# Kernel optimization log

Hardware: AMD Instinct MI355X
Metric: run time of the kernel (lower is better)

Reference implementation:

```python
import jax, jax.numpy as jnp
import numpy as np
import math

B, H, W, C = 8, 112, 112, 192
WS, SHIFT, NH = 7, 3, 6
HD = C // NH
N = WS * WS
NW = (H // WS) * (W // WS)
MLP_HID = 4 * C
LOG100 = math.log(100.0)


def _rel_table():
    ch = np.arange(-(WS - 1), WS, dtype=np.float32)
    t = np.stack(np.meshgrid(ch, ch, indexing='ij')).transpose(1, 2, 0).reshape(-1, 2)
    t = t / float(WS - 1) * 8.0
    t = np.sign(t) * np.log2(np.abs(t) + 1.0) / np.log2(8.0)
    return t.astype(np.float32)  # ((2*WS-1)^2, 2)


def _rel_index():
    coords = np.stack(np.meshgrid(np.arange(WS), np.arange(WS), indexing='ij')).reshape(2, -1)
    rel = (coords[:, :, None] - coords[:, None, :]).transpose(1, 2, 0)
    rel = rel + np.array([WS - 1, WS - 1])
    rel = rel * np.array([2 * WS - 1, 1])
    return rel.sum(-1).astype(np.int32)  # (N, N)


def _attn_mask():
    img = np.zeros((H, W), dtype=np.float32)
    cnt = 0
    for hsl in (slice(0, -WS), slice(-WS, -SHIFT), slice(-SHIFT, None)):
        for wsl in (slice(0, -WS), slice(-WS, -SHIFT), slice(-SHIFT, None)):
            img[hsl, wsl] = cnt
            cnt += 1
    mw = img.reshape(H // WS, WS, W // WS, WS).transpose(0, 2, 1, 3).reshape(-1, N)
    diff = mw[:, None, :] - mw[:, :, None]
    return np.where(diff != 0, -100.0, 0.0).astype(np.float32)  # (NW, N, N)

REL_TABLE = jnp.asarray(_rel_table())
REL_INDEX = jnp.asarray(_rel_index())
ATTN_MASK = jnp.asarray(_attn_mask())


def _ln(v, g, b, eps=1e-5):
    m = jnp.mean(v, axis=-1, keepdims=True)
    s = jnp.mean((v - m) ** 2, axis=-1, keepdims=True)
    return (v - m) / jnp.sqrt(s + eps) * g + b


def setup_inputs() -> dict:
    key = jax.random.key(0)
    ks = jax.random.split(key, 12)
    std = 0.02
    inp = {
        'x': jax.random.normal(ks[0], (B, H * W, C), jnp.float32),
        'q_w': jax.random.normal(ks[1], (C, C), jnp.float32) * std,
        'q_b': jnp.zeros((C,), jnp.float32),
        'k_w': jax.random.normal(ks[2], (C, C), jnp.float32) * std,
        'v_w': jax.random.normal(ks[3], (C, C), jnp.float32) * std,
        'v_b': jnp.zeros((C,), jnp.float32),
        'proj_w': jax.random.normal(ks[4], (C, C), jnp.float32) * std,
        'proj_b': jnp.zeros((C,), jnp.float32),
        'logit_scale': jnp.log(10.0 * jnp.ones((NH, 1, 1), jnp.float32)),
        'cpb_w0': jax.random.normal(ks[5], (2, 512), jnp.float32) * std,
        'cpb_b0': jnp.zeros((512,), jnp.float32),
        'cpb_w1': jax.random.normal(ks[6], (512, NH), jnp.float32) * std,
        'ln1_g': jnp.ones((C,), jnp.float32),
        'ln1_b': jnp.zeros((C,), jnp.float32),
        'ln2_g': jnp.ones((C,), jnp.float32),
        'ln2_b': jnp.zeros((C,), jnp.float32),
        'fc1_w': jax.random.normal(ks[7], (C, MLP_HID), jnp.float32) * std,
        'fc1_b': jnp.zeros((MLP_HID,), jnp.float32),
        'fc2_w': jax.random.normal(ks[8], (MLP_HID, C), jnp.float32) * std,
        'fc2_b': jnp.zeros((C,), jnp.float32),
    }
    return inp


def reference(x, q_w, q_b, k_w, v_w, v_b, proj_w, proj_b, logit_scale,
              cpb_w0, cpb_b0, cpb_w1, ln1_g, ln1_b, ln2_g, ln2_b,
              fc1_w, fc1_b, fc2_w, fc2_b):
    shortcut = x  # (B, L, C)
    h = x.reshape(B, H, W, C)
    # cyclic shift
    h = jnp.roll(h, shift=(-SHIFT, -SHIFT), axis=(1, 2))
    # window partition -> (B*NW, N, C)
    h = h.reshape(B, H // WS, WS, W // WS, WS, C).transpose(0, 1, 3, 2, 4, 5)
    h = h.reshape(B * NW, N, C)

    q = (h @ q_w + q_b).reshape(-1, N, NH, HD).transpose(0, 2, 1, 3)
    k = (h @ k_w).reshape(-1, N, NH, HD).transpose(0, 2, 1, 3)
    v = (h @ v_w + v_b).reshape(-1, N, NH, HD).transpose(0, 2, 1, 3)

    # cosine-similarity attention
    q = q / jnp.maximum(jnp.linalg.norm(q, axis=-1, keepdims=True), 1e-6)
    k = k / jnp.maximum(jnp.linalg.norm(k, axis=-1, keepdims=True), 1e-6)
    scale = jnp.exp(jnp.minimum(logit_scale, LOG100))  # (NH,1,1)
    attn = jnp.einsum('bhqd,bhkd->bhqk', q, k) * scale

    # relative position bias via CPB MLP
    rpb = jax.nn.relu(REL_TABLE @ cpb_w0 + cpb_b0) @ cpb_w1  # (169, NH)
    rpb = rpb[REL_INDEX.reshape(-1)].reshape(N, N, NH).transpose(2, 0, 1)
    rpb = 16.0 * jax.nn.sigmoid(rpb)  # (NH, N, N)
    attn = attn + rpb[None]

    # shift mask
    attn = attn.reshape(B, NW, NH, N, N) + ATTN_MASK[None, :, None]
    attn = attn.reshape(B * NW, NH, N, N)
    attn = jax.nn.softmax(attn, axis=-1)

    out = jnp.einsum('bhqk,bhkd->bhqd', attn, v)
    out = out.transpose(0, 2, 1, 3).reshape(B * NW, N, C)
    out = out @ proj_w + proj_b

    # window reverse + reverse shift
    out = out.reshape(B, H // WS, W // WS, WS, WS, C).transpose(0, 1, 3, 2, 4, 5)
    out = out.reshape(B, H, W, C)
    out = jnp.roll(out, shift=(SHIFT, SHIFT), axis=(1, 2)).reshape(B, H * W, C)

    # post-norm residual (Swin-v2)
    h1 = shortcut + _ln(out, ln1_g, ln1_b)
    mlp = jax.nn.gelu(h1 @ fc1_w + fc1_b) @ fc2_w + fc2_b
    return h1 + _ln(mlp, ln2_g, ln2_b)
```

## Files before the change

### kernel.cpp

```cpp
#include <hip/hip_runtime.h>

typedef unsigned short u16;
typedef unsigned int   u32;
typedef __attribute__((ext_vector_type(8))) short bf16x8;
typedef __attribute__((ext_vector_type(4))) float f32x4;

#define B_      8
#define HW_     112
#define C_      192
#define NH_     6
#define HD_     32
#define L_      (HW_*HW_)
#define M_      (B_*L_)
#define MLP_    768
#define QKVN_   576
#define LOG100_ 4.6051702f
#define LOG2E_  1.44269504f

__device__ __forceinline__ float bf2f(u16 u){
  union { float f; u32 i; } v; v.i = ((u32)u) << 16; return v.f;
}
__device__ __forceinline__ u16 f2bf(float f){
  union { float f; u32 i; } v; v.f = f;
  u32 r = (v.i + 0x7fffu + ((v.i >> 16) & 1u)) >> 16;
  return (u16)r;
}
__device__ __forceinline__ u32 cvtpk(float a, float b){
  u32 r;
  asm("v_cvt_pk_bf16_f32 %0, %1, %2" : "=v"(r) : "v"(a), "v"(b));
  return r;
}
__device__ __forceinline__ void u4_to_f8(uint4 u, float* f){
  f[0]=bf2f((u16)(u.x&0xffffu)); f[1]=bf2f((u16)(u.x>>16));
  f[2]=bf2f((u16)(u.y&0xffffu)); f[3]=bf2f((u16)(u.y>>16));
  f[4]=bf2f((u16)(u.z&0xffffu)); f[5]=bf2f((u16)(u.z>>16));
  f[6]=bf2f((u16)(u.w&0xffffu)); f[7]=bf2f((u16)(u.w>>16));
}

__device__ __forceinline__ int rowelem(int b, int wh, int ww, int t){
  int i = t/7, j = t - i*7;
  int oi = wh*7 + i + 3; if (oi >= 112) oi -= 112;
  int oj = ww*7 + j + 3; if (oj >= 112) oj -= 112;
  return b*L_ + oi*112 + oj;
}

__global__ __launch_bounds__(256) void prep_weights(
    const float* __restrict__ qw, const float* __restrict__ qb,
    const float* __restrict__ kw, const float* __restrict__ vw,
    const float* __restrict__ vb, const float* __restrict__ pw,
    const float* __restrict__ pb, const float* __restrict__ f1w,
    const float* __restrict__ f1b, const float* __restrict__ f2w,
    const float* __restrict__ f2b,
    u16* __restrict__ wt_qkv, float* __restrict__ b_qkv,
    u16* __restrict__ wt_p,   float* __restrict__ b_p,
    u16* __restrict__ wt_f1,  float* __restrict__ b_f1,
    u16* __restrict__ wt_f2,  float* __restrict__ b_f2)
{
  const int S1 = 110592, S2 = 147456, S3 = 294912, S4 = 442368, TOT = 444096;
  int i = blockIdx.x*256 + threadIdx.x;
  if (i >= TOT) return;
  if (i < S1) {
    int n = i/192, k = i%192;
    float v = (n<192) ? qw[k*192+n] : ((n<384) ? kw[k*192+(n-192)] : vw[k*192+(n-384)]);
    wt_qkv[i] = f2bf(v);
  } else if (i < S2) {
    int j = i - S1; int n = j/192, k = j%192;
    wt_p[j] = f2bf(pw[k*192+n]);
  } else if (i < S3) {
    int j = i - S2; int n = j/192, k = j%192;
    wt_f1[j] = f2bf(f1w[k*768+n]);
  } else if (i < S4) {
    int j = i - S3; int n = j/768, k = j%768;
    wt_f2[j] = f2bf(f2w[k*192+n]);
  } else {
    int j = i - S4;
    if (j < 576)        b_qkv[j] = (j<192) ? qb[j] : ((j<384) ? 0.f : vb[j-384]);
    else if (j < 768)   b_p[j-576]   = pb[j-576];
    else if (j < 1536)  b_f1[j-768]  = f1b[j-768];
    else                b_f2[j-1536] = f2b[j-1536];
  }
}

__device__ __forceinline__ float reltab(float x){
  float v = x * (8.f/6.f);
  float r = __log2f(fabsf(v) + 1.f) * (1.f/3.f);
  return (v < 0.f) ? -r : r;
}

__global__ __launch_bounds__(64) void rpb_a_kernel(
    const float* __restrict__ w0, const float* __restrict__ b0,
    const float* __restrict__ w1, float* __restrict__ rpb169)
{
  int tt = blockIdx.x, lane = threadIdx.x;
  float t0 = reltab((float)(tt/13 - 6));
  float t1 = reltab((float)(tt%13 - 6));
  float acc[6] = {0.f,0.f,0.f,0.f,0.f,0.f};
  for (int j = lane; j < 512; j += 64){
    float hid = fmaxf(t0*w0[j] + t1*w0[512+j] + b0[j], 0.f);
#pragma unroll
    for (int h=0; h<6; h++) acc[h] += hid * w1[j*6+h];
  }
#pragma unroll
  for (int h=0; h<6; h++){
#pragma unroll
    for (int m=32; m>=1; m>>=1) acc[h] += __shfl_xor(acc[h], m);
  }
  if (lane == 0){
#pragma unroll
    for (int h=0; h<6; h++) rpb169[tt*6+h] = acc[h];
  }
}

__global__ __launch_bounds__(256) void rpb_b_kernel(
    const float* __restrict__ rpb169, float* __restrict__ biasQ)
{
  int i = blockIdx.x*256 + threadIdx.x;
  if (i >= 98304) return;
  int j = i & 63, q = (i >> 6) & 63;
  int rest = i >> 12;
  int hh = rest % 6, type = rest / 6;
  int kt = j >> 4, s = j & 15;
  int key = ((kt>>1)<<5) + ((s>>2)<<3) + ((kt&1)<<2) + (s&3);
  float val;
  if (key >= 49) val = -60000.f;
  else if (q >= 49) val = 0.f;
  else {
    int qi = q/7, qj = q%7, ki = key/7, kj = key%7;
    int idx = (qi - ki + 6)*13 + (qj - kj + 6);
    float x = rpb169[idx*6 + hh];
    float sig = 16.f / (1.f + __expf(-x));
    int th = type >> 1, tw = type & 1;
    int rq = (th ? (qi<4?1:2) : 0)*3 + (tw ? (qj<4?1:2) : 0);
    int rk = (th ? (ki<4?1:2) : 0)*3 + (tw ? (kj<4?1:2) : 0);
    float msk = (rq != rk) ? -100.f : 0.f;
    val = (sig + msk) * LOG2E_;
  }
  biasQ[i] = val;
}

__device__ __forceinline__ float fast_gelu(float v){
  float t = v*v;
  float w = v * fmaf(-0.1029432f, t, -2.30220817f);
  float e = exp2f(w);
  return v * __builtin_amdgcn_rcpf(1.f + e);
}

#define MODE_GELU 0
#define MODE_LN1  1
#define MODE_LN2  2

template<int K, int MODE>
__global__ __launch_bounds__(512,4) void gemm_fused(
    const u16* __restrict__ A, const u16* __restrict__ Wt,
    const float* __restrict__ bias,
    const float* __restrict__ lng, const float* __restrict__ lnb,
    const float* __restrict__ base32, const u16* __restrict__ base16,
    u16* __restrict__ out16, float* __restrict__ out32, int NN)
{
  __shared__ __align__(16) u16 lds[20480];
  const int tid  = threadIdx.x;
  const int wave = tid >> 6, lane = tid & 63;
  const int m0 = blockIdx.x * 128;
  const int n0 = blockIdx.y * 192;
  const int wr = wave >> 1, wc = wave & 1;
  const int lrow = lane >> 2, lslot = lane & 3;
  const int gk = (lslot ^ ((lrow >> 1) & 3)) * 8;

  const u16* gsrc[3]; u32 ldst[3]; const int nst = (wave < 4) ? 3 : 2;
#pragma unroll
  for (int t=0; t<3; t++){
    int c = wave + t*8;
    if (c < 8)       { gsrc[t] = A  + (size_t)(m0 + c*16 + lrow)*K + gk;      ldst[t] = (u32)(c*512); }
    else if (c < 20) { gsrc[t] = Wt + (size_t)(n0 + (c-8)*16 + lrow)*K + gk;  ldst[t] = (u32)(4096 + (c-8)*512); }
    else             { gsrc[t] = A; ldst[t] = 0; }
  }
  const int lr16 = lane & 15;
  const int lg   = lane >> 4;
  const int slot8 = (lg ^ ((lr16 >> 1) & 3)) * 8;
  u32 aoff[2], boff[6];
#pragma unroll
  for (int mt=0; mt<2; mt++) aoff[mt] = (u32)((wr*32 + mt*16 + lr16)*32 + slot8);
#pragma unroll
  for (int nt=0; nt<6; nt++) boff[nt] = (u32)(4096 + (wc*96 + nt*16 + lr16)*32 + slot8);

  f32x4 acc[2][6];
#pragma unroll
  for (int mt=0; mt<2; mt++)
#pragma unroll
    for (int nt=0; nt<6; nt++)
      acc[mt][nt] = (f32x4){0.f,0.f,0.f,0.f};

  const int NT = K/32;
#define STAGE_F(tt, ph) do { \
  _Pragma("unroll") \
  for (int s_=0; s_<3; s_++) if (s_ < nst) \
    __builtin_amdgcn_global_load_lds( \
        (const __attribute__((address_space(1))) void*)(gsrc[s_] + (tt)*32), \
        (__attribute__((address_space(3))) void*)&lds[ldst[s_] + (ph)], 16, 0, 0); \
} while(0)

  STAGE_F(0, 0u);
  __syncthreads();
  for (int t=0; t<NT; t++){
    const u32 pb = (u32)(t&1)*10240u;
    if (t+1 < NT) STAGE_F(t+1, pb ^ 10240u);
    bf16x8 af[2], bf[6];
#pragma unroll
    for (int mt=0; mt<2; mt++) af[mt] = *(const bf16x8*)&lds[pb + aoff[mt]];
#pragma unroll
    for (int nt=0; nt<6; nt++) bf[nt] = *(const bf16x8*)&lds[pb + boff[nt]];
#pragma unroll
    for (int mt=0; mt<2; mt++)
#pragma unroll
      for (int nt=0; nt<6; nt++)
        acc[mt][nt] = __builtin_amdgcn_mfma_f32_16x16x32_bf16(af[mt], bf[nt], acc[mt][nt], 0, 0, 0);
    __syncthreads();
  }
#undef STAGE_F

#pragma unroll
  for (int nt=0; nt<6; nt++){
    float bsv = bias[n0 + wc*96 + nt*16 + lr16];
#pragma unroll
    for (int mt=0; mt<2; mt++)
#pragma unroll
      for (int r2=0; r2<4; r2++) acc[mt][nt][r2] += bsv;
  }

  if (MODE == MODE_GELU){
#pragma unroll
    for (int mt=0; mt<2; mt++){
      int rbase = m0 + wr*32 + mt*16 + lg*4;
#pragma unroll
      for (int nt=0; nt<6; nt++){
        int col = n0 + wc*96 + nt*16 + lr16;
#pragma unroll
        for (int r2=0; r2<4; r2++)
          out16[(size_t)(rbase + r2)*NN + col] = f2bf(fast_gelu(acc[mt][nt][r2]));
      }
    }
  } else {
    float sv[2][4], sq[2][4];
#pragma unroll
    for (int mt=0; mt<2; mt++)
#pragma unroll
      for (int r2=0; r2<4; r2++){
        float s=0.f, q=0.f;
#pragma unroll
        for (int nt=0; nt<6; nt++){ float x = acc[mt][nt][r2]; s += x; q += x*x; }
        sv[mt][r2]=s; sq[mt][r2]=q;
      }
#pragma unroll
    for (int d=1; d<16; d<<=1){
#pragma unroll
      for (int mt=0; mt<2; mt++)
#pragma unroll
        for (int r2=0; r2<4; r2++){
          sv[mt][r2] += __shfl_xor(sv[mt][r2], d);
          sq[mt][r2] += __shfl_xor(sq[mt][r2], d);
        }
    }
    float* red = (float*)lds;
    if (lr16 == 0){
#pragma unroll
      for (int mt=0; mt<2; mt++)
#pragma unroll
        for (int r2=0; r2<4; r2++){
          int row = wr*32 + mt*16 + lg*4 + r2;
          red[row*4 + wc*2]     = sv[mt][r2];
          red[row*4 + wc*2 + 1] = sq[mt][r2];
        }
    }
    __syncthreads();
    float mean[2][4], rstd[2][4];
#pragma unroll
    for (int mt=0; mt<2; mt++)
#pragma unroll
      for (int r2=0; r2<4; r2++){
        int row = wr*32 + mt*16 + lg*4 + r2;
        float s = red[row*4] + red[row*4+2];
        float q = red[row*4+1] + red[row*4+3];
        float m = s*(1.f/192.f);
        float v = fmaxf(q*(1.f/192.f) - m*m, 0.f);
        mean[mt][r2] = m; rstd[mt][r2] = rsqrtf(v + 1e-5f);
      }
    float gg[6], be[6];
#pragma unroll
    for (int nt=0; nt<6; nt++){
      int col = n0 + wc*96 + nt*16 + lr16;
      gg[nt] = lng[col]; be[nt] = lnb[col];
    }
#pragma unroll
    for (int mt=0; mt<2; mt++){
      int rbase = m0 + wr*32 + mt*16 + lg*4;
#pragma unroll
      for (int nt=0; nt<6; nt++){
        int col = n0 + wc*96 + nt*16 + lr16;
#pragma unroll
        for (int r2=0; r2<4; r2++){
          size_t idx = (size_t)(rbase + r2)*192 + col;
          float r = (acc[mt][nt][r2] - mean[mt][r2])*rstd[mt][r2]*gg[nt] + be[nt];
          if (MODE == MODE_LN1){
            r += base32[idx];
            out16[idx] = f2bf(r);
          } else {
            r += bf2f(base16[idx]);
            out32[idx] = r;
          }
        }
      }
    }
  }
}

__global__ __launch_bounds__(512,4) void gemm_qkv_kernel(
    const float* __restrict__ X, const u16* __restrict__ Wt,
    const float* __restrict__ bias, u16* __restrict__ out)
{
  __shared__ __align__(16) u16 lds[20480];
  const int tid  = threadIdx.x;
  const int wave = tid >> 6, lane = tid & 63;
  const int m0 = blockIdx.x * 128;
  const int n0 = blockIdx.y * 192;
  const int wr = wave >> 1, wc = wave & 1;
  const int lrow = lane >> 2, lslot = lane & 3;
  const int gk = (lslot ^ ((lrow >> 1) & 3)) * 8;

  const u16* gsrcB[2]; u32 ldstB[2]; const int nstB = (wave < 4) ? 2 : 1;
#pragma unroll
  for (int t=0; t<2; t++){
    int c = wave + t*8;
    if (c < 12) { gsrcB[t] = Wt + (size_t)(n0 + c*16 + lrow)*192 + gk; ldstB[t] = (u32)(4096 + c*512); }
    else        { gsrcB[t] = Wt; ldstB[t] = 0; }
  }
  const int ar = tid >> 2, as = tid & 3;
  const float* gA = X + (size_t)(m0 + ar)*192 + as*8;
  const u32 dsta = (u32)(ar*32 + (as ^ ((ar >> 1) & 3))*8);

  const int lr16 = lane & 15;
  const int lg   = lane >> 4;
  const int slot8 = (lg ^ ((lr16 >> 1) & 3)) * 8;
  u32 aoff[2], boff[6];
#pragma unroll
  for (int mt=0; mt<2; mt++) aoff[mt] = (u32)((wr*32 + mt*16 + lr16)*32 + slot8);
#pragma unroll
  for (int nt=0; nt<6; nt++) boff[nt] = (u32)(4096 + (wc*96 + nt*16 + lr16)*32 + slot8);

  f32x4 acc[2][6];
#pragma unroll
  for (int mt=0; mt<2; mt++)
#pragma unroll
    for (int nt=0; nt<6; nt++)
      acc[mt][nt] = (f32x4){0.f,0.f,0.f,0.f};

#define STAGE_B(tt, ph) do { \
  _Pragma("unroll") \
  for (int s_=0; s_<2; s_++) if (s_ < nstB) \
    __builtin_amdgcn_global_load_lds( \
        (const __attribute__((address_space(1))) void*)(gsrcB[s_] + (tt)*32), \
        (__attribute__((address_space(3))) void*)&lds[ldstB[s_] + (ph)], 16, 0, 0); \
} while(0)

  {
    float4 a0 = *(const float4*)gA;
    float4 a1 = *(const float4*)(gA + 4);
    STAGE_B(0, 0u);
    uint4 aw;
    aw.x = cvtpk(a0.x, a0.y); aw.y = cvtpk(a0.z, a0.w);
    aw.z = cvtpk(a1.x, a1.y); aw.w = cvtpk(a1.z, a1.w);
    *(uint4*)(void*)&lds[dsta] = aw;
  }
  __syncthreads();

  for (int t=0; t<6; t++){
    const u32 pb = (u32)(t&1)*10240u;
    const u32 pn = pb ^ 10240u;
    float4 a0, a1;
    if (t < 5){
      a0 = *(const float4*)(gA + (t+1)*32);
      a1 = *(const float4*)(gA + (t+1)*32 + 4);
      STAGE_B(t+1, pn);
    }
    bf16x8 af[2], bf[6];
#pragma unroll
    for (int mt=0; mt<2; mt++) af[mt] = *(const bf16x8*)&lds[pb + aoff[mt]];
#pragma unroll
    for (int nt=0; nt<6; nt++) bf[nt] = *(const bf16x8*)&lds[pb + boff[nt]];
#pragma unroll
    for (int mt=0; mt<2; mt++)
#pragma unroll
      for (int nt=0; nt<6; nt++)
        acc[mt][nt] = __builtin_amdgcn_mfma_f32_16x16x32_bf16(af[mt], bf[nt], acc[mt][nt], 0, 0, 0);
    if (t < 5){
      uint4 aw;
      aw.x = cvtpk(a0.x, a0.y); aw.y = cvtpk(a0.z, a0.w);
      aw.z = cvtpk(a1.x, a1.y); aw.w = cvtpk(a1.z, a1.w);
      *(uint4*)(void*)&lds[pn + dsta] = aw;
    }
    __syncthreads();
  }
#undef STAGE_B

#pragma unroll
  for (int mt=0; mt<2; mt++){
    int rbase = m0 + wr*32 + mt*16 + lg*4;
#pragma unroll
    for (int nt=0; nt<6; nt++){
      int col = n0 + wc*96 + nt*16 + lr16;
      float bsv = bias[col];
#pragma unroll
      for (int r2=0; r2<4; r2++)
        out[(size_t)(rbase + r2)*QKVN_ + col] = f2bf(acc[mt][nt][r2] + bsv);
    }
  }
}

__global__ __launch_bounds__(384) void attn_kernel(
    const u16* __restrict__ qkv, const float* __restrict__ lsc,
    const float* __restrict__ biasQ, u16* __restrict__ attn_out)
{
  __shared__ __align__(16) u16 smem[12288];
  const int tid  = threadIdx.x;
  const int wave = tid >> 6;
  const int lane = tid & 63;
  char* smb = (char*)smem + wave*4096;
  const int hh = wave;
  const int w  = blockIdx.x;
  const int b  = w >> 8;
  const int wh = (w >> 4) & 15, ww = w & 15;
  const int lg = lane >> 4, lr = lane & 15;
  const int type = ((wh==15)?2:0) + ((ww==15)?1:0);
  const float qscale = __expf(fminf(lsc[hh], LOG100_)) * LOG2E_;

  union BU { bf16x8 v; u32 u[4]; };

  const int myrow = rowelem(b, wh, ww, min(lane, 48));

  const u16* vsrc = qkv + (size_t)myrow*QKVN_ + 384 + hh*32;
  uint4 vld[4];
#pragma unroll
  for (int r=0; r<4; r++) vld[r] = *(const uint4*)(vsrc + r*8);

  int rowq[4], krow[4];
#pragma unroll
  for (int qt=0; qt<4; qt++) rowq[qt] = __shfl(myrow, qt*16 + lr);
#pragma unroll
  for (int kt=0; kt<4; kt++){
    int sig = ((kt>>1)<<5) + ((lr>>2)<<3) + ((kt&1)<<2) + (lr&3);
    krow[kt] = __shfl(myrow, sig);
  }

  bf16x8 qf[4], kf[4];
#pragma unroll
  for (int qt=0; qt<4; qt++){
    const u16* base = qkv + (size_t)rowq[qt]*QKVN_ + hh*32 + lg*8;
    uint4 u = *(const uint4*)base;
    float f[8]; u4_to_f8(u, f);
    float ss = 0.f;
#pragma unroll
    for (int d=0; d<8; d++) ss += f[d]*f[d];
    ss += __shfl_xor(ss, 16); ss += __shfl_xor(ss, 32);
    float rn = qscale * __builtin_amdgcn_rcpf(fmaxf(sqrtf(ss), 1e-6f));
    BU bu;
#pragma unroll
    for (int p=0; p<4; p++) bu.u[p] = cvtpk(f[2*p]*rn, f[2*p+1]*rn);
    qf[qt] = bu.v;
  }
#pragma unroll
  for (int kt=0; kt<4; kt++){
    const u16* base = qkv + (size_t)krow[kt]*QKVN_ + 192 + hh*32 + lg*8;
    uint4 u = *(const uint4*)base;
    float f[8]; u4_to_f8(u, f);
    float ss = 0.f;
#pragma unroll
    for (int d=0; d<8; d++) ss += f[d]*f[d];
    ss += __shfl_xor(ss, 16); ss += __shfl_xor(ss, 32);
    float rn = __builtin_amdgcn_rcpf(fmaxf(sqrtf(ss), 1e-6f));
    BU bu;
#pragma unroll
    for (int p=0; p<4; p++) bu.u[p] = cvtpk(f[2*p]*rn, f[2*p+1]*rn);
    kf[kt] = bu.v;
  }

  f32x4 s2[4][4];
#pragma unroll
  for (int kt=0; kt<4; kt++)
#pragma unroll
    for (int qt=0; qt<4; qt++)
      s2[kt][qt] = __builtin_amdgcn_mfma_f32_16x16x32_bf16(kf[kt], qf[qt],
                     (f32x4){0.f,0.f,0.f,0.f}, 0, 0, 0);

#pragma unroll
  for (int r=0; r<4; r++){
    u32 wds[4] = {vld[r].x, vld[r].y, vld[r].z, vld[r].w};
#pragma unroll
    for (int i=0; i<8; i++){
      int d = r*8 + i;
      u16 val = (u16)(wds[i>>1] >> ((i&1)*16));
      int addr = (d*128 + lane*2) ^ ((d&7)<<4);
      *(u16*)(smb + addr) = val;
    }
  }

  const float* bq = biasQ + (size_t)(type*6 + hh)*4096;
#pragma unroll
  for (int qt=0; qt<4; qt++){
    int q = qt*16 + lr;
#pragma unroll
    for (int kt=0; kt<4; kt++){
      f32x4 bv = *(const f32x4*)(bq + q*64 + kt*16 + lg*4);
      s2[kt][qt] += bv;
    }
  }
#pragma unroll
  for (int qt=0; qt<4; qt++){
    float m = s2[0][qt][0];
#pragma unroll
    for (int kt=0; kt<4; kt++)
#pragma unroll
      for (int r2=0; r2<4; r2++) m = fmaxf(m, s2[kt][qt][r2]);
    m = fmaxf(m, __shfl_xor(m, 16));
    m = fmaxf(m, __shfl_xor(m, 32));
    float sum = 0.f;
#pragma unroll
    for (int kt=0; kt<4; kt++)
#pragma unroll
      for (int r2=0; r2<4; r2++){
        float e = exp2f(s2[kt][qt][r2] - m);
        s2[kt][qt][r2] = e; sum += e;
      }
    sum += __shfl_xor(sum, 16);
    sum += __shfl_xor(sum, 32);
    float rs = __builtin_amdgcn_rcpf(sum);
#pragma unroll
    for (int kt=0; kt<4; kt++)
#pragma unroll
      for (int r2=0; r2<4; r2++) s2[kt][qt][r2] *= rs;
  }

  __syncthreads();

  f32x4 o2[2][4];
#pragma unroll
  for (int dt=0; dt<2; dt++)
#pragma unroll
    for (int qt=0; qt<4; qt++)
      o2[dt][qt] = (f32x4){0.f,0.f,0.f,0.f};

#pragma unroll
  for (int kb=0; kb<2; kb++){
    bf16x8 af[2];
#pragma unroll
    for (int dt=0; dt<2; dt++){
      int d = dt*16 + lr;
      int addr = (d*128 + kb*64 + lg*16) ^ ((d&7)<<4);
      af[dt] = *(const bf16x8*)(smb + addr);
    }
#pragma unroll
    for (int qt=0; qt<4; qt++){
      BU bu;
      bu.u[0] = cvtpk(s2[2*kb][qt][0],   s2[2*kb][qt][1]);
      bu.u[1] = cvtpk(s2[2*kb][qt][2],   s2[2*kb][qt][3]);
      bu.u[2] = cvtpk(s2[2*kb+1][qt][0], s2[2*kb+1][qt][1]);
      bu.u[3] = cvtpk(s2[2*kb+1][qt][2], s2[2*kb+1][qt][3]);
#pragma unroll
      for (int dt=0; dt<2; dt++)
        o2[dt][qt] = __builtin_amdgcn_mfma_f32_16x16x32_bf16(af[dt], bu.v, o2[dt][qt], 0, 0, 0);
    }
  }

#pragma unroll
  for (int qt=0; qt<4; qt++){
    int q = qt*16 + lr;
    if (q < 49){
      u16* op = attn_out + (size_t)rowq[qt]*C_ + hh*32;
#pragma unroll
      for (int dt=0; dt<2; dt++){
        uint2 u2;
        u2.x = cvtpk(o2[dt][qt][0], o2[dt][qt][1]);
        u2.y = cvtpk(o2[dt][qt][2], o2[dt][qt][3]);
        *(uint2*)(void*)(op + dt*16 + lg*4) = u2;
      }
    }
  }
}

__global__ __launch_bounds__(512,4) void mlp_fused_kernel(
    const u16* __restrict__ h1,
    const u16* __restrict__ wf1,
    const float* __restrict__ bf1,
    const u16* __restrict__ wf2,
    const float* __restrict__ bf2,
    const float* __restrict__ lng, const float* __restrict__ lnb,
    float* __restrict__ out)
{
  __shared__ __align__(16) char smb[75776];
  const int tid  = threadIdx.x;
  const int wave = tid >> 6, lane = tid & 63;
  const int m0 = blockIdx.x * 64;
  const int wr = wave >> 1, wc = wave & 1;
  const int lr16 = lane & 15, lg = lane >> 4;
  const int lrow = lane >> 2, lslot = lane & 3;
  const int gko = (lslot ^ ((lrow >> 1) & 3)) * 8;
  const int slot8 = (lg ^ ((lr16 >> 1) & 3)) * 8;

  {
    const u16* src = h1 + (size_t)m0*192;
#pragma unroll
    for (int j=0; j<3; j++){
      int i = tid + 512*j;
      int row = i/24, c8 = i%24;
      uint4 v = *(const uint4*)(src + i*8);
      *(uint4*)(smb + row*400 + c8*16) = v;
    }
  }

#define STG1(c_, k_, ph_) do { \
  _Pragma("unroll") \
  for (int s_=0; s_<2; s_++){ \
    int ch__ = wave + s_*8; \
    if (ch__ < 12){ \
      const u16* sp__ = wf1 + (size_t)((c_)*192 + ch__*16 + lrow)*192 + (k_)*32 + gko; \
      __builtin_amdgcn_global_load_lds( \
          (const __attribute__((address_space(1))) void*)sp__, \
          (__attribute__((address_space(3))) void*)(smb + (ph_) + ch__*1024), 16, 0, 0); \
    } } } while(0)
#define STG2(c_, k_, ph_) do { \
  _Pragma("unroll") \
  for (int s_=0; s_<2; s_++){ \
    int ch__ = wave + s_*8; \
    if (ch__ < 12){ \
      const u16* sp__ = wf2 + (size_t)(ch__*16 + lrow)*768 + (c_)*192 + (k_)*32 + gko; \
      __builtin_amdgcn_global_load_lds( \
          (const __attribute__((address_space(1))) void*)sp__, \
          (__attribute__((address_space(3))) void*)(smb + (ph_) + ch__*1024), 16, 0, 0); \
    } } } while(0)

  f32x4 oacc[6];
#pragma unroll
  for (int nt=0; nt<6; nt++) oacc[nt] = (f32x4){0.f,0.f,0.f,0.f};

  for (int c=0; c<4; c++){
    f32x4 macc[6];
#pragma unroll
    for (int nt=0; nt<6; nt++) macc[nt] = (f32x4){0.f,0.f,0.f,0.f};

    STG1(c, 0, 51200u);
    __syncthreads();
#pragma unroll
    for (int k=0; k<6; k++){
      u32 pb = 51200u + (u32)(k&1)*12288u;
      if (k < 5) STG1(c, k+1, 51200u + (u32)((k+1)&1)*12288u);
      bf16x8 af = *(const bf16x8*)(smb + ((wr*16 + lr16)*200 + k*32 + lg*8)*2);
      bf16x8 bfv[6];
#pragma unroll
      for (int nt=0; nt<6; nt++)
        bfv[nt] = *(const bf16x8*)(smb + pb + ((wc*96 + nt*16 + lr16)*32 + slot8)*2);
#pragma unroll
      for (int nt=0; nt<6; nt++)
        macc[nt] = __builtin_amdgcn_mfma_f32_16x16x32_bf16(af, bfv[nt], macc[nt], 0, 0, 0);
      __syncthreads();
    }
    STG2(c, 0, 51200u);
#pragma unroll
    for (int nt=0; nt<6; nt++){
      int col = wc*96 + nt*16 + lr16;
      float bsv = bf1[c*192 + col];
#pragma unroll
      for (int r2=0; r2<4; r2++){
        int tok = wr*16 + lg*4 + r2;
        float g = fast_gelu(macc[nt][r2] + bsv);
        *(u16*)(smb + 25600 + (tok*200 + col)*2) = f2bf(g);
      }
    }
    __syncthreads();
#pragma unroll
    for (int k=0; k<6; k++){
      u32 pb = 51200u + (u32)(k&1)*12288u;
      if (k < 5) STG2(c, k+1, 51200u + (u32)((k+1)&1)*12288u);
      bf16x8 af = *(const bf16x8*)(smb + 25600 + ((wr*16 + lr16)*200 + k*32 + lg*8)*2);
      bf16x8 bfv[6];
#pragma unroll
      for (int nt=0; nt<6; nt++)
        bfv[nt] = *(const bf16x8*)(smb + pb + ((wc*96 + nt*16 + lr16)*32 + slot8)*2);
#pragma unroll
      for (int nt=0; nt<6; nt++)
        oacc[nt] = __builtin_amdgcn_mfma_f32_16x16x32_bf16(af, bfv[nt], oacc[nt], 0, 0, 0);
      __syncthreads();
    }
  }
#undef STG1
#undef STG2

#pragma unroll
  for (int nt=0; nt<6; nt++){
    float bsv = bf2[wc*96 + nt*16 + lr16];
#pragma unroll
    for (int r2=0; r2<4; r2++) oacc[nt][r2] += bsv;
  }
  float sv[4], sq[4];
#pragma unroll
  for (int r2=0; r2<4; r2++){
    float s=0.f, q=0.f;
#pragma unroll
    for (int nt=0; nt<6; nt++){ float x = oacc[nt][r2]; s += x; q += x*x; }
    sv[r2]=s; sq[r2]=q;
  }
#pragma unroll
  for (int d=1; d<16; d<<=1){
#pragma unroll
    for (int r2=0; r2<4; r2++){
      sv[r2] += __shfl_xor(sv[r2], d);
      sq[r2] += __shfl_xor(sq[r2], d);
    }
  }
  float* red = (float*)(smb + 51200);
  if (lr16 == 0){
#pragma unroll
    for (int r2=0; r2<4; r2++){
      int row = wr*16 + lg*4 + r2;
      red[row*4 + wc*2]     = sv[r2];
      red[row*4 + wc*2 + 1] = sq[r2];
    }
  }
  __syncthreads();
  float gg[6], be[6];
#pragma unroll
  for (int nt=0; nt<6; nt++){
    int col = wc*96 + nt*16 + lr16;
    gg[nt] = lng[col]; be[nt] = lnb[col];
  }
#pragma unroll
  for (int r2=0; r2<4; r2++){
    int row = wr*16 + lg*4 + r2;
    float s = red[row*4] + red[row*4+2];
    float q = red[row*4+1] + red[row*4+3];
    float mean = s*(1.f/192.f);
    float var  = fmaxf(q*(1.f/192.f) - mean*mean, 0.f);
    float rstd = rsqrtf(var + 1e-5f);
#pragma unroll
    for (int nt=0; nt<6; nt++){
      int col = wc*96 + nt*16 + lr16;
      float base = bf2f(*(const u16*)(smb + (row*200 + col)*2));
      out[(size_t)(m0 + row)*192 + col] = base + (oacc[nt][r2] - mean)*rstd*gg[nt] + be[nt];
    }
  }
}

extern "C" void kernel_launch(void* const* d_in, const int* in_sizes, int n_in,
                              void* d_out, int out_size, void* d_ws, size_t ws_size,
                              hipStream_t stream)
{
  (void)in_sizes; (void)n_in; (void)out_size; (void)ws_size;
  const float* x      = (const float*)d_in[0];
  const float* q_w    = (const float*)d_in[1];
  const float* q_b    = (const float*)d_in[2];
  const float* k_w    = (const float*)d_in[3];
  const float* v_w    = (const float*)d_in[4];
  const float* v_b    = (const float*)d_in[5];
  const float* proj_w = (const float*)d_in[6];
  const float* proj_b = (const float*)d_in[7];
  const float* lsc    = (const float*)d_in[8];
  const float* cpb_w0 = (const float*)d_in[9];
  const float* cpb_b0 = (const float*)d_in[10];
  const float* cpb_w1 = (const float*)d_in[11];
  const float* ln1_g  = (const float*)d_in[12];
  const float* ln1_b  = (const float*)d_in[13];
  const float* ln2_g  = (const float*)d_in[14];
  const float* ln2_b  = (const float*)d_in[15];
  const float* fc1_w  = (const float*)d_in[16];
  const float* fc1_b  = (const float*)d_in[17];
  const float* fc2_w  = (const float*)d_in[18];
  const float* fc2_b  = (const float*)d_in[19];

  char* ws = (char*)d_ws;
  size_t o = 0;
  u16* qkvb = (u16*)(ws + o);    o += 154140672;
  u16* attn_o = (u16*)(ws + o);
  u16* h1b    = attn_o;          o += 38535168;
  u16* wt_qkv = (u16*)(ws + o);  o += 221184;
  float* b_qkv= (float*)(ws + o);o += 2304;
  u16* wt_p   = (u16*)(ws + o);  o += 73728;
  float* b_p  = (float*)(ws + o);o += 768;
  u16* wt_f1  = (u16*)(ws + o);  o += 294912;
  float* b_f1 = (float*)(ws + o);o += 3072;
  u16* wt_f2  = (u16*)(ws + o);  o += 294912;
  float* b_f2 = (float*)(ws + o);o += 768;
  float* rpb169 = (float*)(ws + o); o += 4096;
  float* biasQ  = (float*)(ws + o); o += 393216;

  prep_weights<<<1735, 256, 0, stream>>>(q_w, q_b, k_w, v_w, v_b, proj_w, proj_b,
      fc1_w, fc1_b, fc2_w, fc2_b, wt_qkv, b_qkv, wt_p, b_p, wt_f1, b_f1, wt_f2, b_f2);
  rpb_a_kernel<<<169, 64, 0, stream>>>(cpb_w0, cpb_b0, cpb_w1, rpb169);
  rpb_b_kernel<<<384, 256, 0, stream>>>(rpb169, biasQ);

  gemm_qkv_kernel<<<dim3(784,3), 512, 0, stream>>>(x, wt_qkv, b_qkv, qkvb);
  attn_kernel<<<2048, 384, 0, stream>>>(qkvb, lsc, biasQ, attn_o);
  gemm_fused<192, MODE_LN1><<<dim3(784,1), 512, 0, stream>>>(
      attn_o, wt_p, b_p, ln1_g, ln1_b, x, nullptr, h1b, nullptr, 192);
  mlp_fused_kernel<<<1568, 512, 0, stream>>>(
      h1b, wt_f1, b_f1, wt_f2, b_f2, ln2_g, ln2_b, (float*)d_out);
}
```

Before: 304.7 us.

## Load MLP weight fragments directly from global memory instead of LDS staging

The fused MLP kernel no longer stages fc1/fc2 weight tiles into shared memory with global_load_lds double-buffering. Each wave now reads its B fragments straight from global memory, relying on L2/cache since all blocks share the same weights. This removes many per-k-step barriers and shrinks the LDS footprint, which may allow more resident blocks. In exchange, each wave issues uncoalesced, latency-exposed global loads inside the MFMA loop with no prefetch.

```diff
diff --git a/kernel.cpp b/kernel.cpp
--- a/kernel.cpp
+++ b/kernel.cpp
@@ -594,15 +594,12 @@
     const float* __restrict__ lng, const float* __restrict__ lnb,
     float* __restrict__ out)
 {
-  __shared__ __align__(16) char smb[75776];
+  __shared__ __align__(16) char smb[52224];
   const int tid  = threadIdx.x;
   const int wave = tid >> 6, lane = tid & 63;
   const int m0 = blockIdx.x * 64;
   const int wr = wave >> 1, wc = wave & 1;
   const int lr16 = lane & 15, lg = lane >> 4;
-  const int lrow = lane >> 2, lslot = lane & 3;
-  const int gko = (lslot ^ ((lrow >> 1) & 3)) * 8;
-  const int slot8 = (lg ^ ((lr16 >> 1) & 3)) * 8;
 
   {
     const u16* src = h1 + (size_t)m0*192;
@@ -614,27 +611,10 @@
       *(uint4*)(smb + row*400 + c8*16) = v;
     }
   }
-
-#define STG1(c_, k_, ph_) do { \
-  _Pragma("unroll") \
-  for (int s_=0; s_<2; s_++){ \
-    int ch__ = wave + s_*8; \
-    if (ch__ < 12){ \
-      const u16* sp__ = wf1 + (size_t)((c_)*192 + ch__*16 + lrow)*192 + (k_)*32 + gko; \
-      __builtin_amdgcn_global_load_lds( \
-          (const __attribute__((address_space(1))) void*)sp__, \
-          (__attribute__((address_space(3))) void*)(smb + (ph_) + ch__*1024), 16, 0, 0); \
-    } } } while(0)
-#define STG2(c_, k_, ph_) do { \
-  _Pragma("unroll") \
-  for (int s_=0; s_<2; s_++){ \
-    int ch__ = wave + s_*8; \
-    if (ch__ < 12){ \
-      const u16* sp__ = wf2 + (size_t)(ch__*16 + lrow)*768 + (c_)*192 + (k_)*32 + gko; \
-      __builtin_amdgcn_global_load_lds( \
-          (const __attribute__((address_space(1))) void*)sp__, \
-          (__attribute__((address_space(3))) void*)(smb + (ph_) + ch__*1024), 16, 0, 0); \
-    } } } while(0)
+  __syncthreads();
+
+  const u16* w1b = wf1 + (size_t)(wc*96 + lr16)*192 + lg*8;
+  const u16* w2b = wf2 + (size_t)(wc*96 + lr16)*768 + lg*8;
 
   f32x4 oacc[6];
 #pragma unroll
@@ -644,24 +624,19 @@
     f32x4 macc[6];
 #pragma unroll
     for (int nt=0; nt<6; nt++) macc[nt] = (f32x4){0.f,0.f,0.f,0.f};
-
-    STG1(c, 0, 51200u);
-    __syncthreads();
+    const u16* w1c = w1b + (size_t)c*36864;
 #pragma unroll
     for (int k=0; k<6; k++){
-      u32 pb = 51200u + (u32)(k&1)*12288u;
-      if (k < 5) STG1(c, k+1, 51200u + (u32)((k+1)&1)*12288u);
       bf16x8 af = *(const bf16x8*)(smb + ((wr*16 + lr16)*200 + k*32 + lg*8)*2);
       bf16x8 bfv[6];
 #pragma unroll
       for (int nt=0; nt<6; nt++)
-        bfv[nt] = *(const bf16x8*)(smb + pb + ((wc*96 + nt*16 + lr16)*32 + slot8)*2);
+        bfv[nt] = *(const bf16x8*)(w1c + nt*3072 + k*32);
 #pragma unroll
       for (int nt=0; nt<6; nt++)
         macc[nt] = __builtin_amdgcn_mfma_f32_16x16x32_bf16(af, bfv[nt], macc[nt], 0, 0, 0);
-      __syncthreads();
-    }
-    STG2(c, 0, 51200u);
+    }
+    __syncthreads();
 #pragma unroll
     for (int nt=0; nt<6; nt++){
       int col = wc*96 + nt*16 + lr16;
@@ -676,21 +651,16 @@
     __syncthreads();
 #pragma unroll
     for (int k=0; k<6; k++){
-      u32 pb = 51200u + (u32)(k&1)*12288u;
-      if (k < 5) STG2(c, k+1, 51200u + (u32)((k+1)&1)*12288u);
       bf16x8 af = *(const bf16x8*)(smb + 25600 + ((wr*16 + lr16)*200 + k*32 + lg*8)*2);
       bf16x8 bfv[6];
 #pragma unroll
       for (int nt=0; nt<6; nt++)
-        bfv[nt] = *(const bf16x8*)(smb + pb + ((wc*96 + nt*16 + lr16)*32 + slot8)*2);
+        bfv[nt] = *(const bf16x8*)(w2b + nt*12288 + c*192 + k*32);
 #pragma unroll
       for (int nt=0; nt<6; nt++)
         oacc[nt] = __builtin_amdgcn_mfma_f32_16x16x32_bf16(af, bfv[nt], oacc[nt], 0, 0, 0);
-      __syncthreads();
-    }
-  }
-#undef STG1
-#undef STG2
+    }
+  }
 
 #pragma unroll
   for (int nt=0; nt<6; nt++){
@@ -715,6 +685,7 @@
     }
   }
   float* red = (float*)(smb + 51200);
+  __syncthreads();
   if (lr16 == 0){
 #pragma unroll
     for (int r2=0; r2<4; r2++){
```

After: 634.2 us. +108.1%, slower.
